# Performance work log

Measured on AMD Instinct MI355X. Metric: run time of the kernel, lower is better.

## Reference

```python
import jax, jax.numpy as jnp
import numpy as np

B, T, C = 2, 2048, 1024
E, K = 8, 2            # n_experts, top_k (n_experts_active)
H = 2736               # round8(int(4*C*2/3)) SwiGLU hidden dim


def setup_inputs() -> dict:
    key = jax.random.key(0)
    ks = jax.random.split(key, 8)
    def w(k, shape, fan_in):
        return jax.random.normal(k, shape, jnp.float32) * (1.0 / np.sqrt(fan_in))
    x = jax.random.normal(ks[0], (B, T, C), jnp.float32)
    router_w = w(ks[1], (C, E), C)          # gate.weight.T
    wg = w(ks[2], (E, C, H), C)             # stacked expert w_gate.weight.T
    wu = w(ks[3], (E, C, H), C)             # stacked expert w_up.weight.T
    wd = w(ks[4], (E, H, C), H)             # stacked expert w_down.weight.T
    sg = w(ks[5], (C, H), C)                # shared expert gate
    su = w(ks[6], (C, H), C)                # shared expert up
    sd = w(ks[7], (H, C), H)                # shared expert down
    return {"x": x, "router_w": router_w, "wg": wg, "wu": wu, "wd": wd,
            "sg": sg, "su": su, "sd": sd}


def reference(x, router_w, wg, wu, wd, sg, su, sd):
    Bx, Tx, Cx = x.shape
    xf = x.reshape(-1, Cx)                       # (Tk, C)
    Tk = xf.shape[0]

    # --- router ---
    logits = xf @ router_w                       # (Tk, E)
    top_v, top_i = jax.lax.top_k(logits, K)      # (Tk, K)
    rw = jax.nn.softmax(top_v, axis=-1)          # normalized weights over selected

    # combine weights per (token, expert): scatter router weights
    rows = jnp.arange(Tk)[:, None]
    w_te = jnp.zeros((Tk, E), xf.dtype).at[rows, top_i].add(rw)   # (Tk, E)

    # --- experts (dense dispatch; weight w_te zeros out unselected experts) ---
    gate = jnp.einsum('tc,ech->teh', xf, wg)     # (Tk, E, H)
    up = jnp.einsum('tc,ech->teh', xf, wu)
    h = jax.nn.silu(gate) * up                   # SwiGLU hidden
    out = jnp.einsum('teh,te,ehc->tc', h, w_te, wd)   # weighted combine

    # --- shared expert ---
    out = out + (jax.nn.silu(xf @ sg) * (xf @ su)) @ sd

    # --- aux load-balancing loss ---
    mask = jnp.zeros((Tk, E), xf.dtype).at[rows, top_i].add(1.0)
    f = mask.mean(axis=0) / K
    p = jax.nn.softmax(logits, axis=-1).mean(axis=0)
    aux_loss = E * (f * p).sum()

    return out.reshape(Bx, Tx, Cx), aux_loss
```

## Files before the change

### kernel.cpp

```cpp
#include <hip/hip_runtime.h>

typedef _Float16 f16;
typedef _Float16 f16x4 __attribute__((ext_vector_type(4)));
typedef _Float16 f16x8 __attribute__((ext_vector_type(8)));
typedef float f32x4 __attribute__((ext_vector_type(4)));

#define TK 4096
#define CD 1024
#define HD 2736
#define HP 2816
#define MT 104
#define RC 13312

#define GLDS16(ldsp, gp) __builtin_amdgcn_global_load_lds( \
    (const __attribute__((address_space(1))) unsigned int*)(gp), \
    (__attribute__((address_space(3))) unsigned int*)(ldsp), 16, 0, 0)

static constexpr size_t WS_XB  = 0;
static constexpr size_t WS_H   = WS_XB  + (size_t)TK*CD*2;
static constexpr size_t WS_WGT = WS_H   + (size_t)RC*HP*2;
static constexpr size_t WS_WUT = WS_WGT + (size_t)8*HP*CD*2;
static constexpr size_t WS_WDT = WS_WUT + (size_t)8*HP*CD*2;
static constexpr size_t WS_SGT = WS_WDT + (size_t)8*CD*HP*2;
static constexpr size_t WS_SUT = WS_SGT + (size_t)HP*CD*2;
static constexpr size_t WS_SDT = WS_SUT + (size_t)HP*CD*2;
static constexpr size_t WS_CT  = WS_SDT + (size_t)CD*HP*2;
static constexpr size_t CT_STOK = 0;
static constexpr size_t CT_SW   = CT_STOK + (size_t)RC*4;
static constexpr size_t CT_TI   = CT_SW   + (size_t)RC*4;
static constexpr size_t CT_TW   = CT_TI   + (size_t)TK*2*4;
static constexpr size_t CT_CNT  = CT_TW   + (size_t)TK*2*4;
static constexpr size_t CT_PS   = CT_CNT  + 32;
static constexpr size_t CT_CUR  = CT_PS   + 32;
static constexpr size_t CT_OFF  = CT_CUR  + 32;
static constexpr size_t CT_SIZE = CT_OFF  + 64;

__global__ void k_xb(const float* __restrict__ x, f16* __restrict__ xb) {
    int i = (blockIdx.x * 256 + threadIdx.x) * 4;
    float4 v = *(const float4*)(x + i);
    f16x4 o = { (f16)v.x, (f16)v.y, (f16)v.z, (f16)v.w };
    *(f16x4*)(xb + i) = o;
}

__global__ __launch_bounds__(256) void k_tr(const float* __restrict__ src, f16* __restrict__ dst,
                     int R, int Cc, int Rp, int Cp,
                     size_t sstride, size_t dstride) {
    src += (size_t)blockIdx.z * sstride;
    dst += (size_t)blockIdx.z * dstride;
    const int tid = threadIdx.x;
    const int l = tid & 63, w = tid >> 6;
    const int cc0 = blockIdx.x * 128 + w * 32 + (l >> 3) * 4;
    const int rr0 = blockIdx.y * 64 + (l & 7) * 8;
    float4 v[8];
    #pragma unroll
    for (int e = 0; e < 8; e++) {
        int gr = rr0 + e;
        if (gr < R && cc0 + 3 < Cc) {
            v[e] = *(const float4*)(src + (size_t)gr * Cc + cc0);
        } else {
            float* ve = (float*)&v[e];
            #pragma unroll
            for (int c = 0; c < 4; c++)
                ve[c] = (gr < R && cc0 + c < Cc) ? src[(size_t)gr * Cc + cc0 + c] : 0.f;
        }
    }
    #pragma unroll
    for (int c = 0; c < 4; c++) {
        const float* vp = (const float*)v;
        f16x8 o = { (f16)vp[0*4+c], (f16)vp[1*4+c], (f16)vp[2*4+c], (f16)vp[3*4+c],
                    (f16)vp[4*4+c], (f16)vp[5*4+c], (f16)vp[6*4+c], (f16)vp[7*4+c] };
        *(f16x8*)(dst + (size_t)(cc0 + c) * Rp + rr0) = o;
    }
}

__global__ void k_router(const float* __restrict__ x, const float* __restrict__ rw,
                         int* __restrict__ topi, float* __restrict__ topw,
                         int* __restrict__ cnt, float* __restrict__ psum) {
    __shared__ float pl[8];
    int tid = threadIdx.x;
    if (tid < 8) pl[tid] = 0.f;
    __syncthreads();
    int wave = tid >> 6, lane = tid & 63;
    int t = blockIdx.x * 4 + wave;
    float acc[8];
    #pragma unroll
    for (int e = 0; e < 8; e++) acc[e] = 0.f;
    const float* xr = x + (size_t)t * CD;
    for (int i = 0; i < CD / 64; i++) {
        int c = lane + i * 64;
        float xv = xr[c];
        const float* wr = rw + c * 8;
        #pragma unroll
        for (int e = 0; e < 8; e++) acc[e] = fmaf(xv, wr[e], acc[e]);
    }
    #pragma unroll
    for (int e = 0; e < 8; e++) {
        #pragma unroll
        for (int off = 32; off; off >>= 1) acc[e] += __shfl_xor(acc[e], off);
    }
    if (lane == 0) {
        float v1 = -1e30f; int i1 = 0;
        #pragma unroll
        for (int e = 0; e < 8; e++) if (acc[e] > v1) { v1 = acc[e]; i1 = e; }
        float v2 = -1e30f; int i2 = (i1 == 0) ? 1 : 0;
        #pragma unroll
        for (int e = 0; e < 8; e++) if (e != i1 && acc[e] > v2) { v2 = acc[e]; i2 = e; }
        float b = expf(v2 - v1);
        float w1 = 1.f / (1.f + b);
        topi[t*2] = i1; topi[t*2+1] = i2;
        topw[t*2] = w1; topw[t*2+1] = b * w1;
        atomicAdd(&cnt[i1], 1);
        atomicAdd(&cnt[i2], 1);
        float m = acc[0];
        #pragma unroll
        for (int e = 1; e < 8; e++) m = fmaxf(m, acc[e]);
        float pe[8]; float s = 0.f;
        #pragma unroll
        for (int e = 0; e < 8; e++) { pe[e] = expf(acc[e] - m); s += pe[e]; }
        float inv = 1.f / s;
        #pragma unroll
        for (int e = 0; e < 8; e++) atomicAdd(&pl[e], pe[e] * inv);
    }
    __syncthreads();
    if (tid < 8) atomicAdd(&psum[tid], pl[tid]);
}

__global__ void k_prefix(const int* __restrict__ cnt, int* __restrict__ cur,
                         int* __restrict__ offs) {
    if (threadIdx.x == 0 && blockIdx.x == 0) {
        int off = 0;
        for (int e = 0; e < 8; e++) {
            offs[e] = off; cur[e] = off;
            off += (cnt[e] + 127) & ~127;
        }
        offs[8] = off;
        offs[9] = RC;
    }
}

__global__ void k_scatter(const int* __restrict__ topi, const float* __restrict__ topw,
                          int* __restrict__ cur, const int* __restrict__ offs,
                          int* __restrict__ stok, float* __restrict__ sw) {
    int t = blockIdx.x * 256 + threadIdx.x;
    if (t >= TK) return;
    #pragma unroll
    for (int s = 0; s < 2; s++) {
        int e = topi[t*2 + s];
        int pos = atomicAdd(&cur[e], 1);
        stok[pos] = t;
        sw[pos] = topw[t*2 + s];
    }
    int base = offs[8];
    stok[base + t] = t;
    sw[base + t] = 1.0f;
}

__global__ __launch_bounds__(256, 2) void k_ffn1(
    const f16* __restrict__ xb, const f16* __restrict__ wgt,
    const f16* __restrict__ wut, const f16* __restrict__ sgt,
    const f16* __restrict__ sut, const int* __restrict__ offs,
    const int* __restrict__ cnt, const int* __restrict__ stok,
    f16* __restrict__ hbuf)
{
    __shared__ f16 As[128*32];
    __shared__ f16 Bg[128*32];
    __shared__ f16 Bu[128*32];

    const int n0 = blockIdx.x * 128;
    const int m0 = blockIdx.y * 128;
    int g = 0;
    while (g < 8 && m0 >= offs[g+1]) g++;
    if (m0 >= offs[8] + TK) return;
    if (g < 8 && (m0 - offs[g]) >= cnt[g]) return;

    const f16* __restrict__ Wg = (g < 8) ? wgt + (size_t)g * HP * CD : sgt;
    const f16* __restrict__ Wu = (g < 8) ? wut + (size_t)g * HP * CD : sut;

    const int tid = threadIdx.x;
    const int lane = tid & 63;
    const int w = tid >> 6;
    const int r0  = w * 32 + (lane >> 2);
    const int kof = (lane & 3) * 8;
    const f16* pa0 = xb + (size_t)stok[m0 + r0]      * CD + kof;
    const f16* pa1 = xb + (size_t)stok[m0 + r0 + 16] * CD + kof;
    const f16* pg0 = Wg + (size_t)(n0 + r0)      * CD + kof;
    const f16* pg1 = Wg + (size_t)(n0 + r0 + 16) * CD + kof;
    const f16* pu0 = Wu + (size_t)(n0 + r0)      * CD + kof;
    const f16* pu1 = Wu + (size_t)(n0 + r0 + 16) * CD + kof;
    f16* const lA = As + w * 1024;
    f16* const lG = Bg + w * 1024;
    f16* const lU = Bu + w * 1024;

    f32x4 accg[4][4], accu[4][4];
    #pragma unroll
    for (int i = 0; i < 4; i++)
        #pragma unroll
        for (int j = 0; j < 4; j++)
            #pragma unroll
            for (int r = 0; r < 4; r++) { accg[i][j][r] = 0.f; accu[i][j][r] = 0.f; }

    const int wm = (w >> 1) * 64;
    const int wn = (w & 1) * 64;
    const int fm = lane & 15;
    const int fq = lane >> 4;

    for (int k0 = 0; k0 < CD; k0 += 32) {
        GLDS16(lA,       pa0 + k0);
        GLDS16(lA + 512, pa1 + k0);
        GLDS16(lG,       pg0 + k0);
        GLDS16(lG + 512, pg1 + k0);
        GLDS16(lU,       pu0 + k0);
        GLDS16(lU + 512, pu1 + k0);
        __syncthreads();
        f16x8 af[4];
        #pragma unroll
        for (int mi = 0; mi < 4; mi++)
            af[mi] = *(const f16x8*)&As[(wm + mi*16 + fm) * 32 + fq * 8];
        #pragma unroll
        for (int ni = 0; ni < 4; ni++) {
            f16x8 bgf = *(const f16x8*)&Bg[(wn + ni*16 + fm) * 32 + fq * 8];
            f16x8 buf = *(const f16x8*)&Bu[(wn + ni*16 + fm) * 32 + fq * 8];
            #pragma unroll
            for (int mi = 0; mi < 4; mi++) {
                accg[mi][ni] = __builtin_amdgcn_mfma_f32_16x16x32_f16(af[mi], bgf, accg[mi][ni], 0, 0, 0);
                accu[mi][ni] = __builtin_amdgcn_mfma_f32_16x16x32_f16(af[mi], buf, accu[mi][ni], 0, 0, 0);
            }
        }
        __syncthreads();
    }

    #pragma unroll
    for (int mi = 0; mi < 4; mi++) {
        #pragma unroll
        for (int ni = 0; ni < 4; ni++) {
            #pragma unroll
            for (int r = 0; r < 4; r++) {
                int row = m0 + wm + mi*16 + fq*4 + r;
                int col = n0 + wn + ni*16 + fm;
                float gv = accg[mi][ni][r];
                float uv = accu[mi][ni][r];
                float hv = gv / (1.f + __expf(-gv)) * uv;
                hbuf[(size_t)row * HP + col] = (f16)hv;
            }
        }
    }
}

__global__ __launch_bounds__(256, 2) void k_ffn2(
    const f16* __restrict__ hbuf, const f16* __restrict__ wdt,
    const f16* __restrict__ sdt, const int* __restrict__ offs,
    const int* __restrict__ cnt, const int* __restrict__ stok,
    const float* __restrict__ sw, float* __restrict__ out)
{
    __shared__ f16 As[128*32];
    __shared__ f16 Bs[128*32];

    const int n0 = blockIdx.x * 128;
    const int m0 = blockIdx.y * 128;
    int g = 0;
    while (g < 8 && m0 >= offs[g+1]) g++;
    if (m0 >= offs[8] + TK) return;
    if (g < 8 && (m0 - offs[g]) >= cnt[g]) return;
    const f16* __restrict__ W = (g < 8) ? wdt + (size_t)g * CD * HP : sdt;

    const int tid = threadIdx.x;
    const int lane = tid & 63;
    const int w = tid >> 6;
    const int r0  = w * 32 + (lane >> 2);
    const int kof = (lane & 3) * 8;
    const f16* pa0 = hbuf + (size_t)(m0 + r0)      * HP + kof;
    const f16* pa1 = hbuf + (size_t)(m0 + r0 + 16) * HP + kof;
    const f16* pb0 = W + (size_t)(n0 + r0)      * HP + kof;
    const f16* pb1 = W + (size_t)(n0 + r0 + 16) * HP + kof;
    f16* const lA = As + w * 1024;
    f16* const lB = Bs + w * 1024;

    f32x4 acc[4][4];
    #pragma unroll
    for (int i = 0; i < 4; i++)
        #pragma unroll
        for (int j = 0; j < 4; j++)
            #pragma unroll
            for (int r = 0; r < 4; r++) acc[i][j][r] = 0.f;

    const int wm = (w >> 1) * 64;
    const int wn = (w & 1) * 64;
    const int fm = lane & 15;
    const int fq = lane >> 4;

    for (int k0 = 0; k0 < HP; k0 += 32) {
        GLDS16(lA,       pa0 + k0);
        GLDS16(lA + 512, pa1 + k0);
        GLDS16(lB,       pb0 + k0);
        GLDS16(lB + 512, pb1 + k0);
        __syncthreads();
        f16x8 af[4];
        #pragma unroll
        for (int mi = 0; mi < 4; mi++)
            af[mi] = *(const f16x8*)&As[(wm + mi*16 + fm) * 32 + fq * 8];
        #pragma unroll
        for (int ni = 0; ni < 4; ni++) {
            f16x8 bfr = *(const f16x8*)&Bs[(wn + ni*16 + fm) * 32 + fq * 8];
            #pragma unroll
            for (int mi = 0; mi < 4; mi++)
                acc[mi][ni] = __builtin_amdgcn_mfma_f32_16x16x32_f16(af[mi], bfr, acc[mi][ni], 0, 0, 0);
        }
        __syncthreads();
    }

    #pragma unroll
    for (int mi = 0; mi < 4; mi++) {
        #pragma unroll
        for (int r = 0; r < 4; r++) {
            int row = m0 + wm + mi*16 + fq*4 + r;
            int tok = stok[row];
            float wgt = sw[row];
            if (wgt != 0.f) {
                #pragma unroll
                for (int ni = 0; ni < 4; ni++) {
                    int col = n0 + wn + ni*16 + fm;
                    atomicAdd(&out[(size_t)tok * CD + col], wgt * acc[mi][ni][r]);
                }
            }
        }
    }
}

__global__ void k_aux(const int* __restrict__ cnt, const float* __restrict__ psum,
                      float* __restrict__ out_aux) {
    if (threadIdx.x == 0 && blockIdx.x == 0) {
        float a = 0.f;
        for (int e = 0; e < 8; e++) {
            float f = (float)cnt[e] / ((float)TK * 2.f);
            float p = psum[e] / (float)TK;
            a += f * p;
        }
        out_aux[0] = 8.f * a;
    }
}

extern "C" void kernel_launch(void* const* d_in, const int* in_sizes, int n_in,
                              void* d_out, int out_size, void* d_ws, size_t ws_size,
                              hipStream_t stream) {
    const float* x  = (const float*)d_in[0];
    const float* rw = (const float*)d_in[1];
    const float* wg = (const float*)d_in[2];
    const float* wu = (const float*)d_in[3];
    const float* wd = (const float*)d_in[4];
    const float* sg = (const float*)d_in[5];
    const float* su = (const float*)d_in[6];
    const float* sd = (const float*)d_in[7];
    float* out = (float*)d_out;

    char* ws = (char*)d_ws;
    f16* xb   = (f16*)(ws + WS_XB);
    f16* hbuf = (f16*)(ws + WS_H);
    f16* wgt  = (f16*)(ws + WS_WGT);
    f16* wut  = (f16*)(ws + WS_WUT);
    f16* wdt  = (f16*)(ws + WS_WDT);
    f16* sgt  = (f16*)(ws + WS_SGT);
    f16* sut  = (f16*)(ws + WS_SUT);
    f16* sdt  = (f16*)(ws + WS_SDT);
    char* ct  = ws + WS_CT;
    int*   stok = (int*)  (ct + CT_STOK);
    float* swt  = (float*)(ct + CT_SW);
    int*   topi = (int*)  (ct + CT_TI);
    float* topw = (float*)(ct + CT_TW);
    int*   cnt  = (int*)  (ct + CT_CNT);
    float* psum = (float*)(ct + CT_PS);
    int*   cur  = (int*)  (ct + CT_CUR);
    int*   offs = (int*)  (ct + CT_OFF);

    hipMemsetAsync(d_out, 0, (size_t)(TK * CD + 1) * 4, stream);
    hipMemsetAsync(ct, 0, CT_SIZE, stream);

    k_xb<<<dim3(TK * CD / 1024), dim3(256), 0, stream>>>(x, xb);
    k_router<<<dim3(TK / 4), dim3(256), 0, stream>>>(x, rw, topi, topw, cnt, psum);
    k_prefix<<<dim3(1), dim3(64), 0, stream>>>(cnt, cur, offs);
    k_scatter<<<dim3(TK / 256), dim3(256), 0, stream>>>(topi, topw, cur, offs, stok, swt);

    k_tr<<<dim3(HP/128, CD/64, 8), dim3(256), 0, stream>>>(wg, wgt, CD, HD, CD, HP, (size_t)CD*HD, (size_t)HP*CD);
    k_tr<<<dim3(HP/128, CD/64, 8), dim3(256), 0, stream>>>(wu, wut, CD, HD, CD, HP, (size_t)CD*HD, (size_t)HP*CD);
    k_tr<<<dim3(CD/128, HP/64, 8), dim3(256), 0, stream>>>(wd, wdt, HD, CD, HP, CD, (size_t)HD*CD, (size_t)CD*HP);
    k_tr<<<dim3(HP/128, CD/64, 1), dim3(256), 0, stream>>>(sg, sgt, CD, HD, CD, HP, 0, 0);
    k_tr<<<dim3(HP/128, CD/64, 1), dim3(256), 0, stream>>>(su, sut, CD, HD, CD, HP, 0, 0);
    k_tr<<<dim3(CD/128, HP/64, 1), dim3(256), 0, stream>>>(sd, sdt, HD, CD, HP, CD, 0, 0);

    k_ffn1<<<dim3(HP/128, MT), dim3(256), 0, stream>>>(xb, wgt, wut, sgt, sut, offs, cnt, stok, hbuf);
    k_ffn2<<<dim3(CD/128, MT), dim3(256), 0, stream>>>(hbuf, wdt, sdt, offs, cnt, stok, swt, out);
    k_aux<<<dim3(1), dim3(64), 0, stream>>>(cnt, psum, out + (size_t)TK * CD);
}
```

Before: 832.9 us.

## Replace atomic scatter-add with slot buffer plus combine kernel, merge launches

The down-projection kernel now writes each routed row's fp32 result to a staging buffer instead of atomically adding into the output. A new per-token combine kernel gathers the two expert slots and the shared-expert row and applies the router weights with FMAs, so the output memset is no longer needed. The staging buffer reuses the gate-weight workspace, which is dead once the first FFN has run. The fp16 conversion of x is folded into the router kernel, and the shared-expert weight transposes are merged into the expert transpose launches as an extra z slice. This adds about 54 MB of staging writes and reads in exchange for removing global atomics and several launches.

```diff
diff --git a/kernel.cpp b/kernel.cpp
--- a/kernel.cpp
+++ b/kernel.cpp
@@ -25,28 +25,30 @@
 static constexpr size_t WS_SUT = WS_SGT + (size_t)HP*CD*2;
 static constexpr size_t WS_SDT = WS_SUT + (size_t)HP*CD*2;
 static constexpr size_t WS_CT  = WS_SDT + (size_t)CD*HP*2;
+static constexpr size_t WS_OBUF = WS_WGT;
 static constexpr size_t CT_STOK = 0;
 static constexpr size_t CT_SW   = CT_STOK + (size_t)RC*4;
 static constexpr size_t CT_TI   = CT_SW   + (size_t)RC*4;
 static constexpr size_t CT_TW   = CT_TI   + (size_t)TK*2*4;
-static constexpr size_t CT_CNT  = CT_TW   + (size_t)TK*2*4;
+static constexpr size_t CT_ISL  = CT_TW   + (size_t)TK*2*4;
+static constexpr size_t CT_CNT  = CT_ISL  + (size_t)TK*2*4;
 static constexpr size_t CT_PS   = CT_CNT  + 32;
 static constexpr size_t CT_CUR  = CT_PS   + 32;
 static constexpr size_t CT_OFF  = CT_CUR  + 32;
 static constexpr size_t CT_SIZE = CT_OFF  + 64;
 
-__global__ void k_xb(const float* __restrict__ x, f16* __restrict__ xb) {
-    int i = (blockIdx.x * 256 + threadIdx.x) * 4;
-    float4 v = *(const float4*)(x + i);
-    f16x4 o = { (f16)v.x, (f16)v.y, (f16)v.z, (f16)v.w };
-    *(f16x4*)(xb + i) = o;
-}
-
-__global__ __launch_bounds__(256) void k_tr(const float* __restrict__ src, f16* __restrict__ dst,
-                     int R, int Cc, int Rp, int Cp,
-                     size_t sstride, size_t dstride) {
-    src += (size_t)blockIdx.z * sstride;
-    dst += (size_t)blockIdx.z * dstride;
+__global__ __launch_bounds__(256) void k_tr(
+    const float* __restrict__ srcMain, f16* __restrict__ dstMain,
+    const float* __restrict__ srcSh,   f16* __restrict__ dstSh,
+    int R, int Cc, int Rp, int Cp, int nMain,
+    size_t sstride, size_t dstride) {
+    const float* src; f16* dst;
+    if ((int)blockIdx.z < nMain) {
+        src = srcMain + (size_t)blockIdx.z * sstride;
+        dst = dstMain + (size_t)blockIdx.z * dstride;
+    } else {
+        src = srcSh; dst = dstSh;
+    }
     const int tid = threadIdx.x;
     const int l = tid & 63, w = tid >> 6;
     const int cc0 = blockIdx.x * 128 + w * 32 + (l >> 3) * 4;
@@ -74,6 +76,7 @@
 }
 
 __global__ void k_router(const float* __restrict__ x, const float* __restrict__ rw,
+                         f16* __restrict__ xb,
                          int* __restrict__ topi, float* __restrict__ topw,
                          int* __restrict__ cnt, float* __restrict__ psum) {
     __shared__ float pl[8];
@@ -86,9 +89,11 @@
     #pragma unroll
     for (int e = 0; e < 8; e++) acc[e] = 0.f;
     const float* xr = x + (size_t)t * CD;
+    f16* xbr = xb + (size_t)t * CD;
     for (int i = 0; i < CD / 64; i++) {
         int c = lane + i * 64;
         float xv = xr[c];
+        xbr[c] = (f16)xv;
         const float* wr = rw + c * 8;
         #pragma unroll
         for (int e = 0; e < 8; e++) acc[e] = fmaf(xv, wr[e], acc[e]);
@@ -140,7 +145,8 @@
 
 __global__ void k_scatter(const int* __restrict__ topi, const float* __restrict__ topw,
                           int* __restrict__ cur, const int* __restrict__ offs,
-                          int* __restrict__ stok, float* __restrict__ sw) {
+                          int* __restrict__ stok, float* __restrict__ sw,
+                          int* __restrict__ islot) {
     int t = blockIdx.x * 256 + threadIdx.x;
     if (t >= TK) return;
     #pragma unroll
@@ -149,6 +155,7 @@
         int pos = atomicAdd(&cur[e], 1);
         stok[pos] = t;
         sw[pos] = topw[t*2 + s];
+        islot[t*2 + s] = pos;
     }
     int base = offs[8];
     stok[base + t] = t;
@@ -249,8 +256,7 @@
 __global__ __launch_bounds__(256, 2) void k_ffn2(
     const f16* __restrict__ hbuf, const f16* __restrict__ wdt,
     const f16* __restrict__ sdt, const int* __restrict__ offs,
-    const int* __restrict__ cnt, const int* __restrict__ stok,
-    const float* __restrict__ sw, float* __restrict__ out)
+    const int* __restrict__ cnt, float* __restrict__ obuf)
 {
     __shared__ f16 As[128*32];
     __shared__ f16 Bs[128*32];
@@ -313,17 +319,34 @@
         #pragma unroll
         for (int r = 0; r < 4; r++) {
             int row = m0 + wm + mi*16 + fq*4 + r;
-            int tok = stok[row];
-            float wgt = sw[row];
-            if (wgt != 0.f) {
-                #pragma unroll
-                for (int ni = 0; ni < 4; ni++) {
-                    int col = n0 + wn + ni*16 + fm;
-                    atomicAdd(&out[(size_t)tok * CD + col], wgt * acc[mi][ni][r]);
-                }
+            #pragma unroll
+            for (int ni = 0; ni < 4; ni++) {
+                int col = n0 + wn + ni*16 + fm;
+                obuf[(size_t)row * CD + col] = acc[mi][ni][r];
             }
         }
     }
+}
+
+__global__ __launch_bounds__(256) void k_comb(
+    const float* __restrict__ obuf, const int* __restrict__ islot,
+    const float* __restrict__ topw, const int* __restrict__ offs,
+    float* __restrict__ out)
+{
+    const int t = blockIdx.x;
+    const int c = threadIdx.x * 4;
+    const int s0 = islot[t*2], s1 = islot[t*2+1];
+    const float w0 = topw[t*2], w1 = topw[t*2+1];
+    const int sh = offs[8] + t;
+    float4 a = *(const float4*)(obuf + (size_t)s0 * CD + c);
+    float4 b = *(const float4*)(obuf + (size_t)s1 * CD + c);
+    float4 s = *(const float4*)(obuf + (size_t)sh * CD + c);
+    float4 o;
+    o.x = fmaf(w0, a.x, fmaf(w1, b.x, s.x));
+    o.y = fmaf(w0, a.y, fmaf(w1, b.y, s.y));
+    o.z = fmaf(w0, a.z, fmaf(w1, b.z, s.z));
+    o.w = fmaf(w0, a.w, fmaf(w1, b.w, s.w));
+    *(float4*)(out + (size_t)t * CD + c) = o;
 }
 
 __global__ void k_aux(const int* __restrict__ cnt, const float* __restrict__ psum,
@@ -361,32 +384,33 @@
     f16* sgt  = (f16*)(ws + WS_SGT);
     f16* sut  = (f16*)(ws + WS_SUT);
     f16* sdt  = (f16*)(ws + WS_SDT);
+    float* obuf = (float*)(ws + WS_OBUF);
     char* ct  = ws + WS_CT;
     int*   stok = (int*)  (ct + CT_STOK);
     float* swt  = (float*)(ct + CT_SW);
     int*   topi = (int*)  (ct + CT_TI);
     float* topw = (float*)(ct + CT_TW);
+    int*   isl  = (int*)  (ct + CT_ISL);
     int*   cnt  = (int*)  (ct + CT_CNT);
     float* psum = (float*)(ct + CT_PS);
     int*   cur  = (int*)  (ct + CT_CUR);
     int*   offs = (int*)  (ct + CT_OFF);
 
-    hipMemsetAsync(d_out, 0, (size_t)(TK * CD + 1) * 4, stream);
     hipMemsetAsync(ct, 0, CT_SIZE, stream);
 
-    k_xb<<<dim3(TK * CD / 1024), dim3(256), 0, stream>>>(x, xb);
-    k_router<<<dim3(TK / 4), dim3(256), 0, stream>>>(x, rw, topi, topw, cnt, psum);
+    k_router<<<dim3(TK / 4), dim3(256), 0, stream>>>(x, rw, xb, topi, topw, cnt, psum);
     k_prefix<<<dim3(1), dim3(64), 0, stream>>>(cnt, cur, offs);
-    k_scatter<<<dim3(TK / 256), dim3(256), 0, stream>>>(topi, topw, cur, offs, stok, swt);
-
-    k_tr<<<dim3(HP/128, CD/64, 8), dim3(256), 0, stream>>>(wg, wgt, CD, HD, CD, HP, (size_t)CD*HD, (size_t)HP*CD);
-    k_tr<<<dim3(HP/128, CD/64, 8), dim3(256), 0, stream>>>(wu, wut, CD, HD, CD, HP, (size_t)CD*HD, (size_t)HP*CD);
-    k_tr<<<dim3(CD/128, HP/64, 8), dim3(256), 0, stream>>>(wd, wdt, HD, CD, HP, CD, (size_t)HD*CD, (size_t)CD*HP);
-    k_tr<<<dim3(HP/128, CD/64, 1), dim3(256), 0, stream>>>(sg, sgt, CD, HD, CD, HP, 0, 0);
-    k_tr<<<dim3(HP/128, CD/64, 1), dim3(256), 0, stream>>>(su, sut, CD, HD, CD, HP, 0, 0);
-    k_tr<<<dim3(CD/128, HP/64, 1), dim3(256), 0, stream>>>(sd, sdt, HD, CD, HP, CD, 0, 0);
+    k_scatter<<<dim3(TK / 256), dim3(256), 0, stream>>>(topi, topw, cur, offs, stok, swt, isl);
+
+    k_tr<<<dim3(HP/128, CD/64, 9), dim3(256), 0, stream>>>(
+        wg, wgt, sg, sgt, CD, HD, CD, HP, 8, (size_t)CD*HD, (size_t)HP*CD);
+    k_tr<<<dim3(HP/128, CD/64, 9), dim3(256), 0, stream>>>(
+        wu, wut, su, sut, CD, HD, CD, HP, 8, (size_t)CD*HD, (size_t)HP*CD);
+    k_tr<<<dim3(CD/128, HP/64, 9), dim3(256), 0, stream>>>(
+        wd, wdt, sd, sdt, HD, CD, HP, CD, 8, (size_t)HD*CD, (size_t)CD*HP);
 
     k_ffn1<<<dim3(HP/128, MT), dim3(256), 0, stream>>>(xb, wgt, wut, sgt, sut, offs, cnt, stok, hbuf);
-    k_ffn2<<<dim3(CD/128, MT), dim3(256), 0, stream>>>(hbuf, wdt, sdt, offs, cnt, stok, swt, out);
+    k_ffn2<<<dim3(CD/128, MT), dim3(256), 0, stream>>>(hbuf, wdt, sdt, offs, cnt, obuf);
+    k_comb<<<dim3(TK), dim3(256), 0, stream>>>(obuf, isl, topw, offs, out);
     k_aux<<<dim3(1), dim3(64), 0, stream>>>(cnt, psum, out + (size_t)TK * CD);
 }
```

Measured after the change: 797.5 us. 1.04x faster.
